# Optimization experiments

Hardware: AMD Instinct MI355X
Metric: run time of the kernel (lower is better)

## Reference

```python
import jax, jax.numpy as jnp
import numpy as np

B, N, D, NFP, L = 4096, 64, 128, 2048, 3  # graphs, nodes/graph, emb_dim, vocab, layers


def setup_inputs() -> dict:
    key = jax.random.key(0)
    k0, k1, k2, k3, k4 = jax.random.split(key, 5)
    fps = jax.random.randint(k0, (B * N,), 0, NFP)            # node fingerprint ids, all graphs concatenated
    adj = jax.random.uniform(k1, (B, N, N), dtype=jnp.float32)  # per-graph adjacency blocks
    emb = jax.random.normal(k2, (NFP, D), dtype=jnp.float32) * 0.02
    W = jax.random.normal(k3, (L, D, D), dtype=jnp.float32) / np.sqrt(D).astype(np.float32)
    b = jax.random.normal(k4, (L, D), dtype=jnp.float32) * 0.01
    return {"fps": fps, "adj": adj, "emb": emb, "W": W, "b": b}


def reference(fps, adj, emb, W, b):
    # h = self.emb(fps): gather, then view as [B, N, D] so the block-diagonal
    # adjs.mm becomes an exact batched matmul over the true graph blocks.
    h = emb[fps].reshape(B, N, D)
    for l in range(L):
        # z = relu(W_l h + b_l); torch Linear is x @ W^T + b
        z = jax.nn.relu(jnp.einsum('bnd,kd->bnk', h, W[l]) + b[l])
        # h = z + adjs.mm(z), restricted to the diagonal blocks (same math)
        h = z + jnp.einsum('bmn,bnd->bmd', adj, z)
    # split by sz_list and sum each chunk -> per-graph sum pooling
    return h.sum(axis=1)  # [B, D]
```

## Files before the change

### kernel.cpp

```cpp
#include <hip/hip_runtime.h>

#define NGRAPH 4096
#define NNODE  64
#define NDIM   128
#define NLAYER 3
#define PH 136
#define PA 72

typedef __attribute__((ext_vector_type(8))) short short8;
typedef __attribute__((ext_vector_type(4))) float f32x4;
typedef __bf16 bf16x2 __attribute__((ext_vector_type(2)));

union S8 { short8 s8; unsigned d[4]; };

static __device__ inline ushort f2bf(float f) {
  unsigned u = __float_as_uint(f);
  u += 0x7FFF + ((u >> 16) & 1);
  return (ushort)(u >> 16);
}

static __device__ inline unsigned pkbf(float x, float y) {
#if __has_builtin(__builtin_amdgcn_cvt_pk_bf16_f32)
  bf16x2 v = __builtin_amdgcn_cvt_pk_bf16_f32(x, y);
  return __builtin_bit_cast(unsigned, v);
#else
  return (unsigned)f2bf(x) | ((unsigned)f2bf(y) << 16);
#endif
}

__device__ __align__(16) ushort g_wbf[NLAYER * NDIM * NDIM];

__global__ __launch_bounds__(256) void convert_w(const float* __restrict__ W) {
  int i = blockIdx.x * 256 + threadIdx.x;
  g_wbf[i] = f2bf(W[i]);
}

__global__ __launch_bounds__(512, 6) void mpnn_mfma(
    const int* __restrict__ fps, const float* __restrict__ adj,
    const float* __restrict__ emb, const float* __restrict__ bias,
    float* __restrict__ out) {
  __shared__ __align__(16) ushort sh0[NNODE * PH];
  __shared__ __align__(16) ushort sh1[NNODE * PH];
  __shared__ __align__(16) ushort sadj[NNODE * PA];

  const int g    = blockIdx.x;
  const int t    = threadIdx.x;
  const int w    = t >> 6;
  const int lane = t & 63;
  const int r    = lane & 15;
  const int q    = lane >> 4;
  const int n0   = w << 4;

  const int addr0 = (r + 32 * (q & 1)) << 2;
  const int addr1 = addr0 + 64;
  const bool hiQ  = (q >= 2);

  const int* fg = fps + g * NNODE;
#pragma unroll
  for (int it = 0; it < 4; ++it) {
    int idx = it * 512 + t;
    int n = idx >> 5;
    int c = (idx & 31) << 2;
    float4 v = *(const float4*)(emb + fg[n] * NDIM + c);
    uint2 u = {pkbf(v.x, v.y), pkbf(v.z, v.w)};
    *(uint2*)(sh0 + n * PH + c) = u;
  }

  const float* adjg = adj + (size_t)g * NNODE * NNODE;
#pragma unroll
  for (int it = 0; it < 2; ++it) {
    int idx = it * 512 + t;
    int n = idx >> 4;
    int c = (idx & 15) << 2;
    float4 v = *(const float4*)(adjg + n * NNODE + c);
    v.x += (n == c + 0) ? 1.0f : 0.0f;
    v.y += (n == c + 1) ? 1.0f : 0.0f;
    v.z += (n == c + 2) ? 1.0f : 0.0f;
    v.w += (n == c + 3) ? 1.0f : 0.0f;
    uint2 u = {pkbf(v.x, v.y), pkbf(v.z, v.w)};
    *(uint2*)(sadj + n * PA + c) = u;
  }

  float bv[NLAYER];
#pragma unroll
  for (int l = 0; l < NLAYER; ++l) bv[l] = bias[l * NDIM + n0 + r];

  __syncthreads();

#pragma unroll 1
  for (int l = 0; l < NLAYER; ++l) {
    const ushort* shr = (l & 1) ? sh1 : sh0;
    ushort*       shw = (l & 1) ? sh0 : sh1;
    const ushort* Wl  = g_wbf + l * NDIM * NDIM;

    f32x4 acc[4];
#pragma unroll
    for (int mt = 0; mt < 4; ++mt) acc[mt] = (f32x4){bv[l], bv[l], bv[l], bv[l]};
#pragma unroll
    for (int k0 = 0; k0 < NDIM; k0 += 32) {
      short8 bw = *(const short8*)(Wl + (n0 + r) * NDIM + k0 + 8 * q);
#pragma unroll
      for (int mt = 0; mt < 4; ++mt) {
        short8 ah = *(const short8*)(shr + (mt * 16 + r) * PH + k0 + 8 * q);
        acc[mt] = __builtin_amdgcn_mfma_f32_16x16x32_bf16(ah, bw, acc[mt], 0, 0, 0);
      }
    }
    unsigned zc[4][2];
#pragma unroll
    for (int mt = 0; mt < 4; ++mt) {
      f32x4 a = acc[mt];
      zc[mt][0] = pkbf(fmaxf(a[0], 0.f), fmaxf(a[1], 0.f));
      zc[mt][1] = pkbf(fmaxf(a[2], 0.f), fmaxf(a[3], 0.f));
    }

    f32x4 acc2[4];
#pragma unroll
    for (int nt = 0; nt < 4; ++nt) acc2[nt] = (f32x4){0.f, 0.f, 0.f, 0.f};
#pragma unroll
    for (int kh = 0; kh < 2; ++kh) {
      S8 az;
#pragma unroll
      for (int p = 0; p < 4; ++p) {
        int comp = p & 1;
        int lo = __builtin_amdgcn_ds_bpermute((p < 2) ? addr0 : addr1,
                                              (int)zc[2 * kh][comp]);
        int hi = __builtin_amdgcn_ds_bpermute((p < 2) ? addr0 : addr1,
                                              (int)zc[2 * kh + 1][comp]);
        az.d[p] = (unsigned)(hiQ ? hi : lo);
      }
#pragma unroll
      for (int nt = 0; nt < 4; ++nt) {
        short8 fb = *(const short8*)(sadj + (nt * 16 + r) * PA + kh * 32 + 8 * q);
        acc2[nt] = __builtin_amdgcn_mfma_f32_16x16x32_bf16(az.s8, fb, acc2[nt], 0, 0, 0);
      }
    }

    if (l < NLAYER - 1) {
#pragma unroll
      for (int nt = 0; nt < 4; ++nt) {
        f32x4 a = acc2[nt];
        uint2 u = {pkbf(a[0], a[1]), pkbf(a[2], a[3])};
        *(uint2*)(shw + (nt * 16 + r) * PH + n0 + 4 * q) = u;
      }
      __syncthreads();
    } else {
      f32x4 s;
#pragma unroll
      for (int i = 0; i < 4; ++i)
        s[i] = acc2[0][i] + acc2[1][i] + acc2[2][i] + acc2[3][i];
#pragma unroll
      for (int m = 1; m <= 8; m <<= 1) {
        s[0] += __shfl_xor(s[0], m);
        s[1] += __shfl_xor(s[1], m);
        s[2] += __shfl_xor(s[2], m);
        s[3] += __shfl_xor(s[3], m);
      }
      if (r == 0) {
        float4 o = {s[0], s[1], s[2], s[3]};
        *(float4*)(out + (size_t)g * NDIM + n0 + 4 * q) = o;
      }
    }
  }
}

extern "C" void kernel_launch(void* const* d_in, const int* in_sizes, int n_in,
                              void* d_out, int out_size, void* d_ws, size_t ws_size,
                              hipStream_t stream) {
  const int*   fps  = (const int*)d_in[0];
  const float* adj  = (const float*)d_in[1];
  const float* emb  = (const float*)d_in[2];
  const float* W    = (const float*)d_in[3];
  const float* bias = (const float*)d_in[4];
  float* out = (float*)d_out;

  hipLaunchKernelGGL(convert_w, dim3(192), dim3(256), 0, stream, W);
  hipLaunchKernelGGL(mpnn_mfma, dim3(NGRAPH), dim3(512), 0, stream,
                     fps, adj, emb, bias, out);
}
```

Before: 163.9 us.

## Halve block to 4 waves, 32 columns per wave, adjacency in registers

Cuts the block to 256 threads, with each wave computing two 16-column output slices so each loaded h fragment is reused across two MFMAs. The adjacency fragments are loaded straight from global memory into registers, and a single shared h buffer replaces the double buffer. A barrier is added before the in-place write-back. This lowers LDS use per block and redundant LDS reads, in exchange for more VGPRs per thread and fewer threads to hide global load latency.

```diff
diff --git a/kernel.cpp b/kernel.cpp
--- a/kernel.cpp
+++ b/kernel.cpp
@@ -5,7 +5,6 @@
 #define NDIM   128
 #define NLAYER 3
 #define PH 136
-#define PA 72
 
 typedef __attribute__((ext_vector_type(8))) short short8;
 typedef __attribute__((ext_vector_type(4))) float f32x4;
@@ -35,13 +34,11 @@
   g_wbf[i] = f2bf(W[i]);
 }
 
-__global__ __launch_bounds__(512, 6) void mpnn_mfma(
+__global__ __launch_bounds__(256, 4) void mpnn_mfma(
     const int* __restrict__ fps, const float* __restrict__ adj,
     const float* __restrict__ emb, const float* __restrict__ bias,
     float* __restrict__ out) {
-  __shared__ __align__(16) ushort sh0[NNODE * PH];
-  __shared__ __align__(16) ushort sh1[NNODE * PH];
-  __shared__ __align__(16) ushort sadj[NNODE * PA];
+  __shared__ __align__(16) ushort sh[NNODE * PH];
 
   const int g    = blockIdx.x;
   const int t    = threadIdx.x;
@@ -49,7 +46,7 @@
   const int lane = t & 63;
   const int r    = lane & 15;
   const int q    = lane >> 4;
-  const int n0   = w << 4;
+  const int n0   = w << 5;
 
   const int addr0 = (r + 32 * (q & 1)) << 2;
   const int addr1 = addr0 + 64;
@@ -57,107 +54,141 @@
 
   const int* fg = fps + g * NNODE;
 #pragma unroll
-  for (int it = 0; it < 4; ++it) {
-    int idx = it * 512 + t;
+  for (int it = 0; it < 8; ++it) {
+    int idx = it * 256 + t;
     int n = idx >> 5;
     int c = (idx & 31) << 2;
     float4 v = *(const float4*)(emb + fg[n] * NDIM + c);
     uint2 u = {pkbf(v.x, v.y), pkbf(v.z, v.w)};
-    *(uint2*)(sh0 + n * PH + c) = u;
+    *(uint2*)(sh + n * PH + c) = u;
   }
 
   const float* adjg = adj + (size_t)g * NNODE * NNODE;
-#pragma unroll
-  for (int it = 0; it < 2; ++it) {
-    int idx = it * 512 + t;
-    int n = idx >> 4;
-    int c = (idx & 15) << 2;
-    float4 v = *(const float4*)(adjg + n * NNODE + c);
-    v.x += (n == c + 0) ? 1.0f : 0.0f;
-    v.y += (n == c + 1) ? 1.0f : 0.0f;
-    v.z += (n == c + 2) ? 1.0f : 0.0f;
-    v.w += (n == c + 3) ? 1.0f : 0.0f;
-    uint2 u = {pkbf(v.x, v.y), pkbf(v.z, v.w)};
-    *(uint2*)(sadj + n * PA + c) = u;
-  }
-
-  float bv[NLAYER];
-#pragma unroll
-  for (int l = 0; l < NLAYER; ++l) bv[l] = bias[l * NDIM + n0 + r];
+  short8 fbr[2][4];
+#pragma unroll
+  for (int kh = 0; kh < 2; ++kh) {
+#pragma unroll
+    for (int nt = 0; nt < 4; ++nt) {
+      int row = nt * 16 + r;
+      int col = kh * 32 + 8 * q;
+      const float* ap = adjg + row * NNODE + col;
+      float4 v0 = *(const float4*)ap;
+      float4 v1 = *(const float4*)(ap + 4);
+      v0.x += (row == col + 0) ? 1.0f : 0.0f;
+      v0.y += (row == col + 1) ? 1.0f : 0.0f;
+      v0.z += (row == col + 2) ? 1.0f : 0.0f;
+      v0.w += (row == col + 3) ? 1.0f : 0.0f;
+      v1.x += (row == col + 4) ? 1.0f : 0.0f;
+      v1.y += (row == col + 5) ? 1.0f : 0.0f;
+      v1.z += (row == col + 6) ? 1.0f : 0.0f;
+      v1.w += (row == col + 7) ? 1.0f : 0.0f;
+      S8 u;
+      u.d[0] = pkbf(v0.x, v0.y);
+      u.d[1] = pkbf(v0.z, v0.w);
+      u.d[2] = pkbf(v1.x, v1.y);
+      u.d[3] = pkbf(v1.z, v1.w);
+      fbr[kh][nt] = u.s8;
+    }
+  }
+
+  float bv[NLAYER][2];
+#pragma unroll
+  for (int l = 0; l < NLAYER; ++l) {
+    bv[l][0] = bias[l * NDIM + n0 + r];
+    bv[l][1] = bias[l * NDIM + n0 + 16 + r];
+  }
 
   __syncthreads();
 
 #pragma unroll 1
   for (int l = 0; l < NLAYER; ++l) {
-    const ushort* shr = (l & 1) ? sh1 : sh0;
-    ushort*       shw = (l & 1) ? sh0 : sh1;
-    const ushort* Wl  = g_wbf + l * NDIM * NDIM;
-
-    f32x4 acc[4];
-#pragma unroll
-    for (int mt = 0; mt < 4; ++mt) acc[mt] = (f32x4){bv[l], bv[l], bv[l], bv[l]};
+    const ushort* Wl = g_wbf + l * NDIM * NDIM;
+
+    f32x4 acc[2][4];
+#pragma unroll
+    for (int s = 0; s < 2; ++s)
+#pragma unroll
+      for (int mt = 0; mt < 4; ++mt)
+        acc[s][mt] = (f32x4){bv[l][s], bv[l][s], bv[l][s], bv[l][s]};
 #pragma unroll
     for (int k0 = 0; k0 < NDIM; k0 += 32) {
-      short8 bw = *(const short8*)(Wl + (n0 + r) * NDIM + k0 + 8 * q);
+      short8 ah[4];
+#pragma unroll
+      for (int mt = 0; mt < 4; ++mt)
+        ah[mt] = *(const short8*)(sh + (mt * 16 + r) * PH + k0 + 8 * q);
+#pragma unroll
+      for (int s = 0; s < 2; ++s) {
+        short8 bw = *(const short8*)(Wl + (n0 + s * 16 + r) * NDIM + k0 + 8 * q);
+#pragma unroll
+        for (int mt = 0; mt < 4; ++mt)
+          acc[s][mt] = __builtin_amdgcn_mfma_f32_16x16x32_bf16(ah[mt], bw, acc[s][mt], 0, 0, 0);
+      }
+    }
+
+    unsigned zc[2][4][2];
+#pragma unroll
+    for (int s = 0; s < 2; ++s)
 #pragma unroll
       for (int mt = 0; mt < 4; ++mt) {
-        short8 ah = *(const short8*)(shr + (mt * 16 + r) * PH + k0 + 8 * q);
-        acc[mt] = __builtin_amdgcn_mfma_f32_16x16x32_bf16(ah, bw, acc[mt], 0, 0, 0);
-      }
-    }
-    unsigned zc[4][2];
-#pragma unroll
-    for (int mt = 0; mt < 4; ++mt) {
-      f32x4 a = acc[mt];
-      zc[mt][0] = pkbf(fmaxf(a[0], 0.f), fmaxf(a[1], 0.f));
-      zc[mt][1] = pkbf(fmaxf(a[2], 0.f), fmaxf(a[3], 0.f));
-    }
-
-    f32x4 acc2[4];
-#pragma unroll
-    for (int nt = 0; nt < 4; ++nt) acc2[nt] = (f32x4){0.f, 0.f, 0.f, 0.f};
-#pragma unroll
-    for (int kh = 0; kh < 2; ++kh) {
-      S8 az;
-#pragma unroll
-      for (int p = 0; p < 4; ++p) {
-        int comp = p & 1;
-        int lo = __builtin_amdgcn_ds_bpermute((p < 2) ? addr0 : addr1,
-                                              (int)zc[2 * kh][comp]);
-        int hi = __builtin_amdgcn_ds_bpermute((p < 2) ? addr0 : addr1,
-                                              (int)zc[2 * kh + 1][comp]);
-        az.d[p] = (unsigned)(hiQ ? hi : lo);
-      }
-#pragma unroll
-      for (int nt = 0; nt < 4; ++nt) {
-        short8 fb = *(const short8*)(sadj + (nt * 16 + r) * PA + kh * 32 + 8 * q);
-        acc2[nt] = __builtin_amdgcn_mfma_f32_16x16x32_bf16(az.s8, fb, acc2[nt], 0, 0, 0);
+        f32x4 a = acc[s][mt];
+        zc[s][mt][0] = pkbf(fmaxf(a[0], 0.f), fmaxf(a[1], 0.f));
+        zc[s][mt][1] = pkbf(fmaxf(a[2], 0.f), fmaxf(a[3], 0.f));
+      }
+
+    f32x4 acc2[2][4];
+#pragma unroll
+    for (int s = 0; s < 2; ++s)
+#pragma unroll
+      for (int nt = 0; nt < 4; ++nt) acc2[s][nt] = (f32x4){0.f, 0.f, 0.f, 0.f};
+#pragma unroll
+    for (int s = 0; s < 2; ++s) {
+#pragma unroll
+      for (int kh = 0; kh < 2; ++kh) {
+        S8 az;
+#pragma unroll
+        for (int p = 0; p < 4; ++p) {
+          int comp = p & 1;
+          int lo = __builtin_amdgcn_ds_bpermute((p < 2) ? addr0 : addr1,
+                                                (int)zc[s][2 * kh][comp]);
+          int hi = __builtin_amdgcn_ds_bpermute((p < 2) ? addr0 : addr1,
+                                                (int)zc[s][2 * kh + 1][comp]);
+          az.d[p] = (unsigned)(hiQ ? hi : lo);
+        }
+#pragma unroll
+        for (int nt = 0; nt < 4; ++nt)
+          acc2[s][nt] = __builtin_amdgcn_mfma_f32_16x16x32_bf16(az.s8, fbr[kh][nt], acc2[s][nt], 0, 0, 0);
       }
     }
 
     if (l < NLAYER - 1) {
-#pragma unroll
-      for (int nt = 0; nt < 4; ++nt) {
-        f32x4 a = acc2[nt];
-        uint2 u = {pkbf(a[0], a[1]), pkbf(a[2], a[3])};
-        *(uint2*)(shw + (nt * 16 + r) * PH + n0 + 4 * q) = u;
-      }
+      __syncthreads();
+#pragma unroll
+      for (int s = 0; s < 2; ++s)
+#pragma unroll
+        for (int nt = 0; nt < 4; ++nt) {
+          f32x4 a = acc2[s][nt];
+          uint2 u = {pkbf(a[0], a[1]), pkbf(a[2], a[3])};
+          *(uint2*)(sh + (nt * 16 + r) * PH + n0 + s * 16 + 4 * q) = u;
+        }
       __syncthreads();
     } else {
-      f32x4 s;
-#pragma unroll
-      for (int i = 0; i < 4; ++i)
-        s[i] = acc2[0][i] + acc2[1][i] + acc2[2][i] + acc2[3][i];
-#pragma unroll
-      for (int m = 1; m <= 8; m <<= 1) {
-        s[0] += __shfl_xor(s[0], m);
-        s[1] += __shfl_xor(s[1], m);
-        s[2] += __shfl_xor(s[2], m);
-        s[3] += __shfl_xor(s[3], m);
-      }
-      if (r == 0) {
-        float4 o = {s[0], s[1], s[2], s[3]};
-        *(float4*)(out + (size_t)g * NDIM + n0 + 4 * q) = o;
+#pragma unroll
+      for (int s = 0; s < 2; ++s) {
+        f32x4 sum;
+#pragma unroll
+        for (int i = 0; i < 4; ++i)
+          sum[i] = acc2[s][0][i] + acc2[s][1][i] + acc2[s][2][i] + acc2[s][3][i];
+#pragma unroll
+        for (int m = 1; m <= 8; m <<= 1) {
+          sum[0] += __shfl_xor(sum[0], m);
+          sum[1] += __shfl_xor(sum[1], m);
+          sum[2] += __shfl_xor(sum[2], m);
+          sum[3] += __shfl_xor(sum[3], m);
+        }
+        if (r == 0) {
+          float4 o = {sum[0], sum[1], sum[2], sum[3]};
+          *(float4*)(out + (size_t)g * NDIM + n0 + s * 16 + 4 * q) = o;
+        }
       }
     }
   }
@@ -174,6 +205,6 @@
   float* out = (float*)d_out;
 
   hipLaunchKernelGGL(convert_w, dim3(192), dim3(256), 0, stream, W);
-  hipLaunchKernelGGL(mpnn_mfma, dim3(NGRAPH), dim3(512), 0, stream,
+  hipLaunchKernelGGL(mpnn_mfma, dim3(NGRAPH), dim3(256), 0, stream,
                      fps, adj, emb, bias, out);
 }
```

New measurement: 182.6 us. 11.4% more time.

## Retile per-layer GEMMs through shared z buffer and keep adjacency in registers

Applied to the files above, without the earlier changes.

Each wave now computes a 16-node by 64-feature tile of the linear layer instead of a 16-feature by 64-node tile. It stages the ReLU output through a transposed shared z buffer rather than exchanging fragments with ds_bpermute. The adjacency fragments are loaded once into registers, which frees their shared memory, and the double-buffered h is replaced by a single buffer. Together these cut LDS use so the launch bounds can target 8 blocks per CU instead of 6. The cost is extra barriers per layer, more W reads per wave, and added register pressure from holding the adjacency.

```diff
diff --git a/kernel.cpp b/kernel.cpp
--- a/kernel.cpp
+++ b/kernel.cpp
@@ -5,13 +5,11 @@
 #define NDIM   128
 #define NLAYER 3
 #define PH 136
-#define PA 72
+#define PZ 72
 
 typedef __attribute__((ext_vector_type(8))) short short8;
 typedef __attribute__((ext_vector_type(4))) float f32x4;
 typedef __bf16 bf16x2 __attribute__((ext_vector_type(2)));
-
-union S8 { short8 s8; unsigned d[4]; };
 
 static __device__ inline ushort f2bf(float f) {
   unsigned u = __float_as_uint(f);
@@ -35,13 +33,12 @@
   g_wbf[i] = f2bf(W[i]);
 }
 
-__global__ __launch_bounds__(512, 6) void mpnn_mfma(
+__global__ __launch_bounds__(512, 8) void mpnn_mfma(
     const int* __restrict__ fps, const float* __restrict__ adj,
     const float* __restrict__ emb, const float* __restrict__ bias,
     float* __restrict__ out) {
-  __shared__ __align__(16) ushort sh0[NNODE * PH];
-  __shared__ __align__(16) ushort sh1[NNODE * PH];
-  __shared__ __align__(16) ushort sadj[NNODE * PA];
+  __shared__ __align__(16) ushort sh[NNODE * PH];
+  __shared__ __align__(16) ushort zbuf[NDIM * PZ];
 
   const int g    = blockIdx.x;
   const int t    = threadIdx.x;
@@ -49,11 +46,9 @@
   const int lane = t & 63;
   const int r    = lane & 15;
   const int q    = lane >> 4;
-  const int n0   = w << 4;
-
-  const int addr0 = (r + 32 * (q & 1)) << 2;
-  const int addr1 = addr0 + 64;
-  const bool hiQ  = (q >= 2);
+  const int mt    = w & 3;
+  const int kbase = (w >> 2) * 64;
+  const int n0    = w << 4;
 
   const int* fg = fps + g * NNODE;
 #pragma unroll
@@ -63,7 +58,7 @@
     int c = (idx & 31) << 2;
     float4 v = *(const float4*)(emb + fg[n] * NDIM + c);
     uint2 u = {pkbf(v.x, v.y), pkbf(v.z, v.w)};
-    *(uint2*)(sh0 + n * PH + c) = u;
+    *(uint2*)(sh + n * PH + c) = u;
   }
 
   const float* adjg = adj + (size_t)g * NNODE * NNODE;
@@ -78,61 +73,56 @@
     v.z += (n == c + 2) ? 1.0f : 0.0f;
     v.w += (n == c + 3) ? 1.0f : 0.0f;
     uint2 u = {pkbf(v.x, v.y), pkbf(v.z, v.w)};
-    *(uint2*)(sadj + n * PA + c) = u;
+    *(uint2*)(zbuf + n * PZ + c) = u;
   }
+  __syncthreads();
 
-  float bv[NLAYER];
+  short8 fbr[2][4];
 #pragma unroll
-  for (int l = 0; l < NLAYER; ++l) bv[l] = bias[l * NDIM + n0 + r];
-
+  for (int kh = 0; kh < 2; ++kh)
+#pragma unroll
+    for (int nt = 0; nt < 4; ++nt)
+      fbr[kh][nt] = *(const short8*)(zbuf + (nt * 16 + r) * PZ + kh * 32 + 8 * q);
   __syncthreads();
 
 #pragma unroll 1
   for (int l = 0; l < NLAYER; ++l) {
-    const ushort* shr = (l & 1) ? sh1 : sh0;
-    ushort*       shw = (l & 1) ? sh0 : sh1;
-    const ushort* Wl  = g_wbf + l * NDIM * NDIM;
+    const ushort* Wl = g_wbf + l * NDIM * NDIM;
+
+    float bv[4];
+#pragma unroll
+    for (int s = 0; s < 4; ++s) bv[s] = bias[l * NDIM + kbase + s * 16 + r];
 
     f32x4 acc[4];
 #pragma unroll
-    for (int mt = 0; mt < 4; ++mt) acc[mt] = (f32x4){bv[l], bv[l], bv[l], bv[l]};
+    for (int s = 0; s < 4; ++s) acc[s] = (f32x4){0.f, 0.f, 0.f, 0.f};
 #pragma unroll
     for (int k0 = 0; k0 < NDIM; k0 += 32) {
-      short8 bw = *(const short8*)(Wl + (n0 + r) * NDIM + k0 + 8 * q);
+      short8 ah = *(const short8*)(sh + (mt * 16 + r) * PH + k0 + 8 * q);
 #pragma unroll
-      for (int mt = 0; mt < 4; ++mt) {
-        short8 ah = *(const short8*)(shr + (mt * 16 + r) * PH + k0 + 8 * q);
-        acc[mt] = __builtin_amdgcn_mfma_f32_16x16x32_bf16(ah, bw, acc[mt], 0, 0, 0);
+      for (int s = 0; s < 4; ++s) {
+        short8 bw = *(const short8*)(Wl + (kbase + s * 16 + r) * NDIM + k0 + 8 * q);
+        acc[s] = __builtin_amdgcn_mfma_f32_16x16x32_bf16(ah, bw, acc[s], 0, 0, 0);
       }
     }
-    unsigned zc[4][2];
+
 #pragma unroll
-    for (int mt = 0; mt < 4; ++mt) {
-      f32x4 a = acc[mt];
-      zc[mt][0] = pkbf(fmaxf(a[0], 0.f), fmaxf(a[1], 0.f));
-      zc[mt][1] = pkbf(fmaxf(a[2], 0.f), fmaxf(a[3], 0.f));
+    for (int s = 0; s < 4; ++s) {
+      uint2 u = {pkbf(fmaxf(acc[s][0] + bv[s], 0.f), fmaxf(acc[s][1] + bv[s], 0.f)),
+                 pkbf(fmaxf(acc[s][2] + bv[s], 0.f), fmaxf(acc[s][3] + bv[s], 0.f))};
+      *(uint2*)(zbuf + (kbase + s * 16 + r) * PZ + mt * 16 + 4 * q) = u;
     }
+    __syncthreads();
 
     f32x4 acc2[4];
 #pragma unroll
     for (int nt = 0; nt < 4; ++nt) acc2[nt] = (f32x4){0.f, 0.f, 0.f, 0.f};
 #pragma unroll
     for (int kh = 0; kh < 2; ++kh) {
-      S8 az;
+      short8 az = *(const short8*)(zbuf + (n0 + r) * PZ + kh * 32 + 8 * q);
 #pragma unroll
-      for (int p = 0; p < 4; ++p) {
-        int comp = p & 1;
-        int lo = __builtin_amdgcn_ds_bpermute((p < 2) ? addr0 : addr1,
-                                              (int)zc[2 * kh][comp]);
-        int hi = __builtin_amdgcn_ds_bpermute((p < 2) ? addr0 : addr1,
-                                              (int)zc[2 * kh + 1][comp]);
-        az.d[p] = (unsigned)(hiQ ? hi : lo);
-      }
-#pragma unroll
-      for (int nt = 0; nt < 4; ++nt) {
-        short8 fb = *(const short8*)(sadj + (nt * 16 + r) * PA + kh * 32 + 8 * q);
-        acc2[nt] = __builtin_amdgcn_mfma_f32_16x16x32_bf16(az.s8, fb, acc2[nt], 0, 0, 0);
-      }
+      for (int nt = 0; nt < 4; ++nt)
+        acc2[nt] = __builtin_amdgcn_mfma_f32_16x16x32_bf16(az, fbr[kh][nt], acc2[nt], 0, 0, 0);
     }
 
     if (l < NLAYER - 1) {
@@ -140,7 +130,7 @@
       for (int nt = 0; nt < 4; ++nt) {
         f32x4 a = acc2[nt];
         uint2 u = {pkbf(a[0], a[1]), pkbf(a[2], a[3])};
-        *(uint2*)(shw + (nt * 16 + r) * PH + n0 + 4 * q) = u;
+        *(uint2*)(sh + (nt * 16 + r) * PH + n0 + 4 * q) = u;
       }
       __syncthreads();
     } else {
```

Result: slower. 327.8 us (+100.0%).
